# Kernel optimization log

Measured on AMD Instinct MI355X. Metric: run time of the kernel, lower is better.

The kernel has to match this reference:

```python
import jax, jax.numpy as jnp
import numpy as np

BIG = 1e10  # large finite value standing in for +inf in masked mins (grad-safe)


def setup_inputs() -> dict:
    key = jax.random.key(0)
    k1, k2, k3 = jax.random.split(key, 3)
    B, C, N = 16, 3, 4096
    x = jax.random.normal(k1, (B, C, N), dtype=jnp.float32)
    y = jax.random.normal(k2, (B, C, N), dtype=jnp.float32)
    mask = jax.random.randint(k3, (B, N), 0, 2, dtype=jnp.int32)
    return {"x": x, "y": y, "mask": mask}


def reference(x, y, mask):
    # x, y: (B, 3, N); mask: (B, N) with 1 = valid point
    xt = jnp.swapaxes(x, 1, 2)  # (B, N, 3)
    yt = jnp.swapaxes(y, 1, 2)  # (B, N, 3)
    xx = jnp.sum(xt * xt, axis=-1)  # (B, N)
    yy = jnp.sum(yt * yt, axis=-1)  # (B, N)
    # squared pairwise distances, P[b, n, m] = ||x_bn - y_bm||^2
    P = xx[:, :, None] + yy[:, None, :] - 2.0 * jnp.einsum("bnd,bmd->bnm", xt, yt)

    valid = mask.astype(bool)                 # (B, N)
    mf = mask.astype(P.dtype)                 # (B, N)
    cnt = jnp.sum(mf, axis=1)                 # (B,) number of valid points per batch

    # direction 1: for each y-point m, min over valid x-rows n; mean over valid m
    mins1 = jnp.min(jnp.where(valid[:, :, None], P, BIG), axis=1)  # (B, N)
    means1 = jnp.sum(mins1 * mf, axis=1) / cnt                      # (B,)

    # direction 2: for each x-point m, min over valid y-cols n; mean over valid m
    mins2 = jnp.min(jnp.where(valid[:, None, :], P, BIG), axis=2)  # (B, N)
    means2 = jnp.sum(mins2 * mf, axis=1) / cnt                      # (B,)

    return jnp.mean(means1) + jnp.mean(means2)
```

## Files before the change

kernel.cpp:

```cpp
#include <hip/hip_runtime.h>

typedef short bf16x8 __attribute__((ext_vector_type(8)));
typedef float f32x16 __attribute__((ext_vector_type(16)));

#define BIG_F 1e10f
constexpr int B = 16;
constexpr int N = 4096;
constexpr int COLS = 512;
constexpr int NCB = N / COLS;
constexpr int PASSES = 2;
constexpr int SUBROWS = 512;
constexpr int NSUB = N / SUBROWS;
constexpr size_t PARTSZ = (size_t)B * NCB * 2 * N;

__device__ __forceinline__ void split(float v, unsigned& h, unsigned& l) {
    unsigned hb = __float_as_uint(v) & 0xFFFF0000u;
    h = hb >> 16;
    float r = v - __uint_as_float(hb);
    l = __float_as_uint(r) >> 16;
}

__device__ __forceinline__ float min3f(float a, float b, float c) {
    return fminf(fminf(a, b), c);
}

__device__ __forceinline__ float4 min4(float4 a, float4 b) {
    return make_float4(fminf(a.x, b.x), fminf(a.y, b.y),
                       fminf(a.z, b.z), fminf(a.w, b.w));
}

#define DPP_MIN(v, ctrl)                                                      \
    v = fminf(v, __int_as_float(__builtin_amdgcn_update_dpp(                  \
            __float_as_int(v), __float_as_int(v), (ctrl), 0xF, 0xF, false)))

__device__ __forceinline__ void rowstyle(float v0, float v1, float v2,
                                         float madd, uint4& w0, uint4& w1) {
    float s = fmaf(v2, v2, fmaf(v1, v1, v0 * v0)) + madd;
    unsigned h0, l0, h1, l1, h2, l2, sh, sl;
    split(-2.0f * v0, h0, l0);
    split(-2.0f * v1, h1, l1);
    split(-2.0f * v2, h2, l2);
    split(s, sh, sl);
    w0 = make_uint4(h0 | (h1 << 16), h2 | (h0 << 16), h1 | (h2 << 16), l0 | (l1 << 16));
    w1 = make_uint4(l2 | (l0 << 16), l1 | (l2 << 16), sh | (sl << 16), 0x3F803F80u);
}
__device__ __forceinline__ void colstyle(float v0, float v1, float v2,
                                         float madd, uint4& w0, uint4& w1) {
    float s = fmaf(v2, v2, fmaf(v1, v1, v0 * v0)) + madd;
    unsigned h0, l0, h1, l1, h2, l2, sh, sl;
    split(v0, h0, l0);
    split(v1, h1, l1);
    split(v2, h2, l2);
    split(s, sh, sl);
    unsigned u0 = h0 | (h1 << 16), u1 = h2 | (l0 << 16), u2 = l1 | (l2 << 16);
    w0 = make_uint4(u0, u1, u2, u0);
    w1 = make_uint4(u1, u2, 0x3F803F80u, sh | (sl << 16));
}

__global__ __launch_bounds__(256, 3) void chamfer_mfma(
    const float* __restrict__ x, const float* __restrict__ y,
    const int* __restrict__ mask,
    float* __restrict__ part,
    float* __restrict__ out)
{
    const int blk  = blockIdx.x;
    const int dir  = blk & 1;
    const int rest = blk >> 1;
    const int b    = rest >> 6;
    const int cb   = (rest >> 3) & 7;
    const int sub  = rest & 7;
    const int t    = threadIdx.x;

    __shared__ __align__(16) unsigned short Bpack[2][COLS][8];

    if (blk == 0 && t == 0) out[0] = 0.0f;

    const float* rsrc = dir ? y : x;
    const float* csrc = dir ? x : y;
    const int*   mb   = mask + b * N;
    const float* rb3  = rsrc + (size_t)b * 3 * N;
    const float* cb3  = csrc + (size_t)b * 3 * N;

#pragma unroll
    for (int i = 0; i < 2; ++i) {
        int c = t + i * 256;
        int m = cb * COLS + c;
        float v0 = cb3[m], v1 = cb3[N + m], v2 = cb3[2 * N + m];
        float madd = mb[m] ? 0.0f : BIG_F;
        uint4 w0, w1;
        if (dir) rowstyle(v0, v1, v2, madd, w0, w1);
        else     colstyle(v0, v1, v2, madd, w0, w1);
        *(uint4*)&Bpack[0][c][0] = w0;
        *(uint4*)&Bpack[1][c][0] = w1;
    }

    const int w    = t >> 6;
    const int L    = t & 63;
    const int half = L >> 5;
    const int lc   = L & 31;

    __syncthreads();

    const unsigned short* Bb = &Bpack[half][lc][0];

    const f32x16 z16 = {0.f,0.f,0.f,0.f,0.f,0.f,0.f,0.f,
                        0.f,0.f,0.f,0.f,0.f,0.f,0.f,0.f};

    auto buildA = [&](int n) -> bf16x8 {
        float v0 = rb3[n], v1 = rb3[N + n], v2 = rb3[2 * N + n];
        float madd = mb[n] ? 0.0f : BIG_F;
        uint4 w0, w1;
        if (dir) colstyle(v0, v1, v2, madd, w0, w1);
        else     rowstyle(v0, v1, v2, madd, w0, w1);
        uint4 wa = half ? w1 : w0;
        return *(bf16x8*)&wa;
    };

    float* pbase = part + (size_t)dir * PARTSZ;

#pragma unroll 1
    for (int pass = 0; pass < PASSES; ++pass) {
        const int rowbase = sub * SUBROWS + pass * 256;
        bf16x8 afrA = buildA(rowbase + w * 32 + lc);
        bf16x8 afrB = buildA(rowbase + 128 + w * 32 + lc);

        float rmA[16], rmB[16];
#pragma unroll
        for (int r = 0; r < 16; ++r) { rmA[r] = 1e30f; rmB[r] = 1e30f; }

#pragma unroll 1
        for (int p = 0; p < 8; ++p) {
            bf16x8 bf0 = *(const bf16x8*)(Bb + p * 512);
            bf16x8 bf1 = *(const bf16x8*)(Bb + p * 512 + 256);
            f32x16 C0a = __builtin_amdgcn_mfma_f32_32x32x16_bf16(afrA, bf0, z16, 0, 0, 0);
            f32x16 C0b = __builtin_amdgcn_mfma_f32_32x32x16_bf16(afrB, bf0, z16, 0, 0, 0);
            f32x16 C1a = __builtin_amdgcn_mfma_f32_32x32x16_bf16(afrA, bf1, z16, 0, 0, 0);
            f32x16 C1b = __builtin_amdgcn_mfma_f32_32x32x16_bf16(afrB, bf1, z16, 0, 0, 0);
#pragma unroll
            for (int r = 0; r < 16; ++r) {
                rmA[r] = min3f(rmA[r], C0a[r], C1a[r]);
                rmB[r] = min3f(rmB[r], C0b[r], C1b[r]);
            }
        }

#pragma unroll
        for (int r = 0; r < 16; ++r) {
            DPP_MIN(rmA[r], 0xB1);   DPP_MIN(rmB[r], 0xB1);
            DPP_MIN(rmA[r], 0x4E);   DPP_MIN(rmB[r], 0x4E);
            DPP_MIN(rmA[r], 0x124);  DPP_MIN(rmB[r], 0x124);
            DPP_MIN(rmA[r], 0x128);  DPP_MIN(rmB[r], 0x128);
        }
        if ((lc & 15) == 0) {
            int sset = lc >> 4;
            float* rpA = pbase + (((size_t)(b * NCB + cb)) * 2 + sset) * N
                       + rowbase + w * 32 + half * 4;
            float* rpB = rpA + 128;
            *(float4*)(rpA +  0) = make_float4(rmA[0],  rmA[1],  rmA[2],  rmA[3]);
            *(float4*)(rpA +  8) = make_float4(rmA[4],  rmA[5],  rmA[6],  rmA[7]);
            *(float4*)(rpA + 16) = make_float4(rmA[8],  rmA[9],  rmA[10], rmA[11]);
            *(float4*)(rpA + 24) = make_float4(rmA[12], rmA[13], rmA[14], rmA[15]);
            *(float4*)(rpB +  0) = make_float4(rmB[0],  rmB[1],  rmB[2],  rmB[3]);
            *(float4*)(rpB +  8) = make_float4(rmB[4],  rmB[5],  rmB[6],  rmB[7]);
            *(float4*)(rpB + 16) = make_float4(rmB[8],  rmB[9],  rmB[10], rmB[11]);
            *(float4*)(rpB + 24) = make_float4(rmB[12], rmB[13], rmB[14], rmB[15]);
        }
    }
}

__global__ __launch_bounds__(256) void finalize_kernel(
    const int* __restrict__ mask,
    const float* __restrict__ part,
    float* __restrict__ out)
{
    const int b = blockIdx.x & 15;
    const int q = blockIdx.x >> 4;
    const int t = threadIdx.x;
    const int* mrow = mask + b * N;

    int cnt = 0;
    for (int i = t; i < N / 4; i += 256) {
        int4 mk = ((const int4*)mrow)[i];
        cnt += mk.x + mk.y + mk.z + mk.w;
    }

    const int p0 = q * 1024 + t * 4;
    const float* d0 = part + (size_t)b * NCB * 2 * N + p0;
    const float* d1 = part + PARTSZ + (size_t)b * NCB * 2 * N + p0;

    float4 rn = *(const float4*)d0;
    float4 mn = *(const float4*)d1;
#pragma unroll 8
    for (int pb = 1; pb < NCB * 2; ++pb) {
        rn = min4(rn, *(const float4*)(d0 + (size_t)pb * N));
        mn = min4(mn, *(const float4*)(d1 + (size_t)pb * N));
    }
    int4 mk = *(const int4*)(mrow + p0);
    float s = (mk.x ? (mn.x + rn.x) : 0.f) + (mk.y ? (mn.y + rn.y) : 0.f)
            + (mk.z ? (mn.z + rn.z) : 0.f) + (mk.w ? (mn.w + rn.w) : 0.f);

    for (int off = 32; off > 0; off >>= 1) {
        s   += __shfl_down(s, off);
        cnt += __shfl_down(cnt, off);
    }
    __shared__ float rs[4];
    __shared__ int   rc[4];
    const int wv = t >> 6;
    if ((t & 63) == 0) { rs[wv] = s; rc[wv] = cnt; }
    __syncthreads();
    if (t == 0) {
        float S = rs[0] + rs[1] + rs[2] + rs[3];
        float C = (float)(rc[0] + rc[1] + rc[2] + rc[3]);
        atomicAdd(out, (S / C) * (1.0f / 16.0f));
    }
}

extern "C" void kernel_launch(void* const* d_in, const int* in_sizes, int n_in,
                              void* d_out, int out_size, void* d_ws, size_t ws_size,
                              hipStream_t stream) {
    const float* x    = (const float*)d_in[0];
    const float* y    = (const float*)d_in[1];
    const int*   mask = (const int*)d_in[2];

    float* part = (float*)d_ws;

    chamfer_mfma<<<dim3(2 * B * NCB * NSUB), 256, 0, stream>>>(
        x, y, mask, part, (float*)d_out);
    finalize_kernel<<<dim3(64), 256, 0, stream>>>(
        mask, part, (float*)d_out);
}
```

Before: 92.42 us.

## Precompute bf16 split operands in a pack kernel and shrink per-job register tiles

Adds a pre-pass kernel that computes the hi/lo bf16-split packed operands for x (row style) and y (column style) once per point and writes them to workspace. The main MFMA kernel then loads these packed fragments directly instead of recomputing the splits for every block, and processes one 32-row tile per job (4 jobs) rather than two tiles per pass. This cuts register pressure so occupancy can be raised from 3 to 6 waves. In exchange it adds an extra kernel launch and workspace traffic, and each job issues fewer independent MFMAs, so there is less instruction-level parallelism per wave.

```diff
diff --git a/kernel.cpp b/kernel.cpp
--- a/kernel.cpp
+++ b/kernel.cpp
@@ -8,7 +8,7 @@
 constexpr int N = 4096;
 constexpr int COLS = 512;
 constexpr int NCB = N / COLS;
-constexpr int PASSES = 2;
+constexpr int JOBS = 4;
 constexpr int SUBROWS = 512;
 constexpr int NSUB = N / SUBROWS;
 constexpr size_t PARTSZ = (size_t)B * NCB * 2 * N;
@@ -57,11 +57,31 @@
     w1 = make_uint4(u1, u2, 0x3F803F80u, sh | (sl << 16));
 }
 
-__global__ __launch_bounds__(256, 3) void chamfer_mfma(
+__global__ __launch_bounds__(256) void pack_kernel(
     const float* __restrict__ x, const float* __restrict__ y,
     const int* __restrict__ mask,
-    float* __restrict__ part,
+    uint4* __restrict__ Txrow, uint4* __restrict__ Tycol,
     float* __restrict__ out)
+{
+    const int idx = blockIdx.x * 256 + threadIdx.x;
+    if (idx == 0) out[0] = 0.0f;
+    const int b  = idx >> 12;
+    const int pt = idx & (N - 1);
+    const float* xb = x + (size_t)b * 3 * N;
+    const float* yb = y + (size_t)b * 3 * N;
+    const float madd = mask[b * N + pt] ? 0.0f : BIG_F;
+    uint4 w0, w1;
+    rowstyle(xb[pt], xb[N + pt], xb[2 * N + pt], madd, w0, w1);
+    Txrow[(size_t)(b * 2 + 0) * N + pt] = w0;
+    Txrow[(size_t)(b * 2 + 1) * N + pt] = w1;
+    colstyle(yb[pt], yb[N + pt], yb[2 * N + pt], madd, w0, w1);
+    Tycol[(size_t)(b * 2 + 0) * N + pt] = w0;
+    Tycol[(size_t)(b * 2 + 1) * N + pt] = w1;
+}
+
+__global__ __launch_bounds__(256, 6) void chamfer_mfma(
+    const uint4* __restrict__ Txrow, const uint4* __restrict__ Tycol,
+    float* __restrict__ part)
 {
     const int blk  = blockIdx.x;
     const int dir  = blk & 1;
@@ -73,25 +93,15 @@
 
     __shared__ __align__(16) unsigned short Bpack[2][COLS][8];
 
-    if (blk == 0 && t == 0) out[0] = 0.0f;
-
-    const float* rsrc = dir ? y : x;
-    const float* csrc = dir ? x : y;
-    const int*   mb   = mask + b * N;
-    const float* rb3  = rsrc + (size_t)b * 3 * N;
-    const float* cb3  = csrc + (size_t)b * 3 * N;
-
-#pragma unroll
-    for (int i = 0; i < 2; ++i) {
-        int c = t + i * 256;
-        int m = cb * COLS + c;
-        float v0 = cb3[m], v1 = cb3[N + m], v2 = cb3[2 * N + m];
-        float madd = mb[m] ? 0.0f : BIG_F;
-        uint4 w0, w1;
-        if (dir) rowstyle(v0, v1, v2, madd, w0, w1);
-        else     colstyle(v0, v1, v2, madd, w0, w1);
-        *(uint4*)&Bpack[0][c][0] = w0;
-        *(uint4*)&Bpack[1][c][0] = w1;
+    const uint4* rowT = dir ? Tycol : Txrow;
+    const uint4* colT = dir ? Txrow : Tycol;
+
+    uint4* Bl = (uint4*)&Bpack[0][0][0];
+    const uint4* Bg = colT + (size_t)b * 2 * N + cb * COLS;
+#pragma unroll
+    for (int k = 0; k < 4; ++k) {
+        int i = t + k * 256;
+        Bl[i] = Bg[(size_t)(i >> 9) * N + (i & 511)];
     }
 
     const int w    = t >> 6;
@@ -102,67 +112,45 @@
     __syncthreads();
 
     const unsigned short* Bb = &Bpack[half][lc][0];
-
     const f32x16 z16 = {0.f,0.f,0.f,0.f,0.f,0.f,0.f,0.f,
                         0.f,0.f,0.f,0.f,0.f,0.f,0.f,0.f};
-
-    auto buildA = [&](int n) -> bf16x8 {
-        float v0 = rb3[n], v1 = rb3[N + n], v2 = rb3[2 * N + n];
-        float madd = mb[n] ? 0.0f : BIG_F;
-        uint4 w0, w1;
-        if (dir) colstyle(v0, v1, v2, madd, w0, w1);
-        else     rowstyle(v0, v1, v2, madd, w0, w1);
-        uint4 wa = half ? w1 : w0;
-        return *(bf16x8*)&wa;
-    };
-
     float* pbase = part + (size_t)dir * PARTSZ;
 
 #pragma unroll 1
-    for (int pass = 0; pass < PASSES; ++pass) {
-        const int rowbase = sub * SUBROWS + pass * 256;
-        bf16x8 afrA = buildA(rowbase + w * 32 + lc);
-        bf16x8 afrB = buildA(rowbase + 128 + w * 32 + lc);
-
-        float rmA[16], rmB[16];
-#pragma unroll
-        for (int r = 0; r < 16; ++r) { rmA[r] = 1e30f; rmB[r] = 1e30f; }
+    for (int jj = 0; jj < JOBS; ++jj) {
+        const int rowbase = sub * SUBROWS + jj * 128;
+        uint4 av = rowT[(size_t)(b * 2 + half) * N + rowbase + w * 32 + lc];
+        bf16x8 afr = *(bf16x8*)&av;
+
+        float rm[16];
+#pragma unroll
+        for (int r = 0; r < 16; ++r) rm[r] = 1e30f;
 
 #pragma unroll 1
         for (int p = 0; p < 8; ++p) {
             bf16x8 bf0 = *(const bf16x8*)(Bb + p * 512);
             bf16x8 bf1 = *(const bf16x8*)(Bb + p * 512 + 256);
-            f32x16 C0a = __builtin_amdgcn_mfma_f32_32x32x16_bf16(afrA, bf0, z16, 0, 0, 0);
-            f32x16 C0b = __builtin_amdgcn_mfma_f32_32x32x16_bf16(afrB, bf0, z16, 0, 0, 0);
-            f32x16 C1a = __builtin_amdgcn_mfma_f32_32x32x16_bf16(afrA, bf1, z16, 0, 0, 0);
-            f32x16 C1b = __builtin_amdgcn_mfma_f32_32x32x16_bf16(afrB, bf1, z16, 0, 0, 0);
-#pragma unroll
-            for (int r = 0; r < 16; ++r) {
-                rmA[r] = min3f(rmA[r], C0a[r], C1a[r]);
-                rmB[r] = min3f(rmB[r], C0b[r], C1b[r]);
-            }
+            f32x16 C0 = __builtin_amdgcn_mfma_f32_32x32x16_bf16(afr, bf0, z16, 0, 0, 0);
+            f32x16 C1 = __builtin_amdgcn_mfma_f32_32x32x16_bf16(afr, bf1, z16, 0, 0, 0);
+#pragma unroll
+            for (int r = 0; r < 16; ++r) rm[r] = min3f(rm[r], C0[r], C1[r]);
         }
 
 #pragma unroll
         for (int r = 0; r < 16; ++r) {
-            DPP_MIN(rmA[r], 0xB1);   DPP_MIN(rmB[r], 0xB1);
-            DPP_MIN(rmA[r], 0x4E);   DPP_MIN(rmB[r], 0x4E);
-            DPP_MIN(rmA[r], 0x124);  DPP_MIN(rmB[r], 0x124);
-            DPP_MIN(rmA[r], 0x128);  DPP_MIN(rmB[r], 0x128);
+            DPP_MIN(rm[r], 0xB1);
+            DPP_MIN(rm[r], 0x4E);
+            DPP_MIN(rm[r], 0x124);
+            DPP_MIN(rm[r], 0x128);
         }
         if ((lc & 15) == 0) {
             int sset = lc >> 4;
-            float* rpA = pbase + (((size_t)(b * NCB + cb)) * 2 + sset) * N
-                       + rowbase + w * 32 + half * 4;
-            float* rpB = rpA + 128;
-            *(float4*)(rpA +  0) = make_float4(rmA[0],  rmA[1],  rmA[2],  rmA[3]);
-            *(float4*)(rpA +  8) = make_float4(rmA[4],  rmA[5],  rmA[6],  rmA[7]);
-            *(float4*)(rpA + 16) = make_float4(rmA[8],  rmA[9],  rmA[10], rmA[11]);
-            *(float4*)(rpA + 24) = make_float4(rmA[12], rmA[13], rmA[14], rmA[15]);
-            *(float4*)(rpB +  0) = make_float4(rmB[0],  rmB[1],  rmB[2],  rmB[3]);
-            *(float4*)(rpB +  8) = make_float4(rmB[4],  rmB[5],  rmB[6],  rmB[7]);
-            *(float4*)(rpB + 16) = make_float4(rmB[8],  rmB[9],  rmB[10], rmB[11]);
-            *(float4*)(rpB + 24) = make_float4(rmB[12], rmB[13], rmB[14], rmB[15]);
+            float* rp = pbase + (((size_t)(b * NCB + cb)) * 2 + sset) * N
+                      + rowbase + w * 32 + half * 4;
+            *(float4*)(rp +  0) = make_float4(rm[0],  rm[1],  rm[2],  rm[3]);
+            *(float4*)(rp +  8) = make_float4(rm[4],  rm[5],  rm[6],  rm[7]);
+            *(float4*)(rp + 16) = make_float4(rm[8],  rm[9],  rm[10], rm[11]);
+            *(float4*)(rp + 24) = make_float4(rm[12], rm[13], rm[14], rm[15]);
         }
     }
 }
@@ -221,10 +209,14 @@
     const float* y    = (const float*)d_in[1];
     const int*   mask = (const int*)d_in[2];
 
-    float* part = (float*)d_ws;
-
+    uint4* Txrow = (uint4*)d_ws;
+    uint4* Tycol = Txrow + (size_t)B * 2 * N;
+    float* part  = (float*)(Tycol + (size_t)B * 2 * N);
+
+    pack_kernel<<<dim3(B * N / 256), 256, 0, stream>>>(
+        x, y, mask, Txrow, Tycol, (float*)d_out);
     chamfer_mfma<<<dim3(2 * B * NCB * NSUB), 256, 0, stream>>>(
-        x, y, mask, part, (float*)d_out);
+        Txrow, Tycol, part);
     finalize_kernel<<<dim3(64), 256, 0, stream>>>(
         mask, part, (float*)d_out);
 }
```

New measurement: 96.83 us. 1.05x slower.
